# Optimization experiments

Hardware: AMD Instinct MI355X
Metric: run time of the kernel (lower is better)

The kernel has to match this reference:

```python
import jax, jax.numpy as jnp
import numpy as np

N = 50000       # nodes
E = 800000      # edges (before self-loops)
IN_DIM = 256
HID = 64
HEADS = 3
N_CLASSES = 40
NEG_SLOPE = 0.2  # PyG GATConv default negative_slope


def setup_inputs() -> dict:
    key = jax.random.key(0)
    ks = jax.random.split(key, 12)
    x = jax.random.normal(ks[0], (N, IN_DIM), jnp.float32)
    src = jax.random.randint(ks[1], (E,), 0, N, dtype=jnp.int32)
    off = jax.random.randint(ks[2], (E,), 1, N, dtype=jnp.int32)
    dst = (src + off) % N  # guarantees no self-loops
    edge_index = jnp.stack([src, dst], axis=0)
    g = 0.1
    W1 = jax.random.normal(ks[3], (IN_DIM, HEADS * HID), jnp.float32) * g
    att_src1 = jax.random.normal(ks[4], (HEADS, HID), jnp.float32) * g
    att_dst1 = jax.random.normal(ks[5], (HEADS, HID), jnp.float32) * g
    b1 = jnp.zeros((HEADS * HID,), jnp.float32)
    W2 = jax.random.normal(ks[6], (HEADS * HID, HEADS * HID), jnp.float32) * g
    att_src2 = jax.random.normal(ks[7], (HEADS, HID), jnp.float32) * g
    att_dst2 = jax.random.normal(ks[8], (HEADS, HID), jnp.float32) * g
    b2 = jnp.zeros((HEADS * HID,), jnp.float32)
    Wout = jax.random.normal(ks[9], (HEADS * HID, N_CLASSES), jnp.float32) * g
    bout = jnp.zeros((N_CLASSES,), jnp.float32)
    return {"x": x, "edge_index": edge_index,
            "W1": W1, "att_src1": att_src1, "att_dst1": att_dst1, "b1": b1,
            "W2": W2, "att_src2": att_src2, "att_dst2": att_dst2, "b2": b2,
            "Wout": Wout, "bout": bout}


def _segment_softmax(logits, seg, num_segments):
    # logits: [E', H], seg: [E'] destination node ids
    m = jax.ops.segment_max(logits, seg, num_segments=num_segments)
    e = jnp.exp(logits - m[seg])
    s = jax.ops.segment_sum(e, seg, num_segments=num_segments)
    return e / s[seg]


def _gat_layer(x, src, dst, W, att_src, att_dst, bias):
    n = x.shape[0]
    h = (x @ W).reshape(n, HEADS, HID)               # lin_src == lin_dst (x is a Tensor)
    a_src = jnp.sum(h * att_src, axis=-1)            # [N, H]
    a_dst = jnp.sum(h * att_dst, axis=-1)            # [N, H]
    alpha = jax.nn.leaky_relu(a_src[src] + a_dst[dst], NEG_SLOPE)  # [E', H]
    alpha = _segment_softmax(alpha, dst, n)
    msg = h[src] * alpha[:, :, None]                 # [E', H, C]
    out = jax.ops.segment_sum(msg, dst, num_segments=n)  # scatter-add aggregate
    return out.reshape(n, HEADS * HID) + bias        # concat heads + bias


def reference(x, edge_index, W1, att_src1, att_dst1, b1,
              W2, att_src2, att_dst2, b2, Wout, bout):
    n = x.shape[0]
    loop = jnp.arange(n, dtype=edge_index.dtype)
    src = jnp.concatenate([edge_index[0], loop])     # add_self_loops=True
    dst = jnp.concatenate([edge_index[1], loop])
    h = _gat_layer(x, src, dst, W1, att_src1, att_dst1, b1)
    h = jax.nn.relu(h)                               # dropout p=0 -> identity
    h = _gat_layer(h, src, dst, W2, att_src2, att_dst2, b2)
    h = jax.nn.relu(h)
    return h @ Wout + bout                           # node-level readout + outlayer
```

## Files before the change

### kernel.cpp

```cpp
#include <hip/hip_runtime.h>
#include <math.h>

#define NN 50000
#define NE 800000
#define KIN 256
#define F 192
#define NH 3
#define NC 40
#define NBLK 49

typedef unsigned short u16;
typedef unsigned int   u32;
typedef __attribute__((ext_vector_type(8))) short bf16x8;
typedef __attribute__((ext_vector_type(4))) float f32x4;

static __device__ __forceinline__ u16 f2bf(float f){
  u32 u = __float_as_uint(f);
  u32 r = (u + 0x7fffu + ((u >> 16) & 1u)) >> 16;
  return (u16)r;
}

__global__ void count_kernel(const int* __restrict__ dst, int* __restrict__ cnt){
  int e = blockIdx.x*256 + threadIdx.x;
  if (e < NE) atomicAdd(&cnt[dst[e]], 1);
}

__global__ __launch_bounds__(256) void partial_kernel(const int* __restrict__ cnt, int* __restrict__ partials){
  __shared__ int red[256];
  const int t = threadIdx.x;
  const int base = blockIdx.x*1024 + t*4;
  int s = 0;
  if (base + 3 < NN){
    int4 v = *(const int4*)&cnt[base];
    s = v.x + v.y + v.z + v.w;
  } else if (base < NN){
    for (int i=base; i<NN; i++) s += cnt[i];
  }
  red[t] = s;
  __syncthreads();
  for (int off=128; off; off>>=1){
    if (t < off) red[t] += red[t+off];
    __syncthreads();
  }
  if (t==0) partials[blockIdx.x] = red[0];
}

__global__ __launch_bounds__(64) void scan_partials(const int* __restrict__ partials,
                                                    int* __restrict__ offsets, int* __restrict__ row_ptr){
  const int lane = threadIdx.x;
  int p = (lane < NBLK)? partials[lane] : 0;
  int inc = p;
  #pragma unroll
  for (int off=1; off<64; off<<=1){
    int v = __shfl_up(inc, off);
    if (lane >= off) inc += v;
  }
  if (lane < NBLK) offsets[lane] = inc - p;
  if (lane == NBLK-1) row_ptr[NN] = inc;
}

__global__ __launch_bounds__(256) void emit_kernel(const int* __restrict__ cnt,
                                                   const int* __restrict__ offsets,
                                                   int* __restrict__ row_ptr){
  __shared__ int ts[256];
  const int t = threadIdx.x;
  const int base = blockIdx.x*1024 + t*4;
  int4 v = make_int4(0,0,0,0);
  if (base + 3 < NN) v = *(const int4*)&cnt[base];
  else if (base < NN){
    v.x = cnt[base];
    if (base+1 < NN) v.y = cnt[base+1];
    if (base+2 < NN) v.z = cnt[base+2];
  }
  int tot = v.x + v.y + v.z + v.w;
  ts[t] = tot;
  __syncthreads();
  #pragma unroll
  for (int off=1; off<256; off<<=1){
    int val = (t >= off)? ts[t-off] : 0;
    __syncthreads();
    ts[t] += val;
    __syncthreads();
  }
  int off0 = offsets[blockIdx.x] + ts[t] - tot;
  if (base < NN)     row_ptr[base]   = off0;
  if (base+1 < NN)   row_ptr[base+1] = off0 + v.x;
  if (base+2 < NN)   row_ptr[base+2] = off0 + v.x + v.y;
  if (base+3 < NN)   row_ptr[base+3] = off0 + v.x + v.y + v.z;
}

__global__ void fill_kernel(const int* __restrict__ src, const int* __restrict__ dst,
                            const int* __restrict__ row_ptr, int* __restrict__ cur,
                            int* __restrict__ col){
  int e = blockIdx.x*256 + threadIdx.x;
  if (e < NE){
    int d = dst[e];
    int p = row_ptr[d] + atomicAdd(&cur[d], 1);
    col[p] = src[e];
  }
}

__global__ void conv_x_kernel(const float* __restrict__ src, u16* __restrict__ dst, int n4){
  int i = blockIdx.x*256 + threadIdx.x;
  if (i < n4){
    float4 v = *(const float4*)&src[(size_t)i*4];
    uint2 p;
    p.x = (u32)f2bf(v.x) | ((u32)f2bf(v.y) << 16);
    p.y = (u32)f2bf(v.z) | ((u32)f2bf(v.w) << 16);
    *(uint2*)&dst[(size_t)i*4] = p;
  }
}

__global__ void conv_wt_kernel(const float* __restrict__ src, u16* __restrict__ dst, int R, int C){
  int e = blockIdx.x*256 + threadIdx.x;
  if (e < R*C){
    int r = e / C, c = e % C;
    dst[(size_t)c*R + r] = f2bf(src[e]);
  }
}

#define SAK 40
template<int K>
__global__ __launch_bounds__(256) void gemm_mfma(const u16* __restrict__ Ab, const u16* __restrict__ Bt,
                                                 u16* __restrict__ C,
                                                 const float* __restrict__ att_src, const float* __restrict__ att_dst,
                                                 float* __restrict__ a_src4, float* __restrict__ a_dst4){
  __shared__ __align__(16) u16 As[64*SAK];
  __shared__ __align__(16) u16 Bs[192*SAK];
  __shared__ float sd_src[64*NH];
  __shared__ float sd_dst[64*NH];
  const int t = threadIdx.x;
  const int wave = t >> 6, lane = t & 63;
  const int quad = lane >> 4, l16 = lane & 15;
  const int r0 = blockIdx.x*64;

  for (int i=t; i<64*NH; i+=256){ sd_src[i]=0.f; sd_dst[i]=0.f; }

  f32x4 acc[4][3];
  #pragma unroll
  for (int rt=0;rt<4;rt++)
    #pragma unroll
    for (int ct=0;ct<3;ct++) acc[rt][ct] = (f32x4){0.f,0.f,0.f,0.f};

  for (int k0=0; k0<K; k0+=32){
    __syncthreads();
    {
      int row = t >> 2, kq = t & 3;
      uint4 v = make_uint4(0,0,0,0);
      if (r0+row < NN) v = *(const uint4*)&Ab[(size_t)(r0+row)*K + k0 + kq*8];
      *(uint4*)&As[row*SAK + kq*8] = v;
    }
    #pragma unroll
    for (int i=0;i<3;i++){
      int idx = t + i*256;
      int n = idx >> 2, kq = idx & 3;
      *(uint4*)&Bs[n*SAK + kq*8] = *(const uint4*)&Bt[(size_t)n*K + k0 + kq*8];
    }
    __syncthreads();
    bf16x8 af[4], bf[3];
    #pragma unroll
    for (int rt=0;rt<4;rt++) af[rt] = *(const bf16x8*)&As[(rt*16 + l16)*SAK + quad*8];
    #pragma unroll
    for (int ct=0;ct<3;ct++) bf[ct] = *(const bf16x8*)&Bs[(wave*48 + ct*16 + l16)*SAK + quad*8];
    #pragma unroll
    for (int rt=0;rt<4;rt++)
      #pragma unroll
      for (int ct=0;ct<3;ct++)
        acc[rt][ct] = __builtin_amdgcn_mfma_f32_16x16x32_bf16(af[rt], bf[ct], acc[rt][ct], 0, 0, 0);
  }

  #pragma unroll
  for (int ct=0;ct<3;ct++){
    const int nbase = wave*48 + ct*16;
    const int n = nbase + l16;
    const int head = nbase >> 6;
    const float as_n = att_src[n], ad_n = att_dst[n];
    #pragma unroll
    for (int rt=0;rt<4;rt++){
      #pragma unroll
      for (int reg=0;reg<4;reg++){
        const int m = rt*16 + quad*4 + reg;
        const float v = acc[rt][ct][reg];
        const int grow = r0 + m;
        if (grow < NN) C[(size_t)grow*F + n] = f2bf(v);
        float ps = v*as_n, pd = v*ad_n;
        #pragma unroll
        for (int off=1; off<16; off<<=1){
          ps += __shfl_xor(ps, off);
          pd += __shfl_xor(pd, off);
        }
        if (l16 == 0){
          atomicAdd(&sd_src[m*NH + head], ps);
          atomicAdd(&sd_dst[m*NH + head], pd);
        }
      }
    }
  }
  __syncthreads();
  if (t < 64){
    int grow = r0 + t;
    if (grow < NN){
      float4 vs = make_float4(sd_src[t*NH+0], sd_src[t*NH+1], sd_src[t*NH+2], 0.f);
      float4 vd = make_float4(sd_dst[t*NH+0], sd_dst[t*NH+1], sd_dst[t*NH+2], 0.f);
      *(float4*)&a_src4[(size_t)grow*4] = vs;
      *(float4*)&a_dst4[(size_t)grow*4] = vd;
    }
  }
}

__global__ __launch_bounds__(256) void gat_agg_wave(const u16* __restrict__ hb,
    const float* __restrict__ a_src4, const float* __restrict__ a_dst4,
    const int* __restrict__ row_ptr, const int* __restrict__ col,
    const float* __restrict__ bias, u16* __restrict__ out){
  __shared__ float s_al[4][64][4];
  const int t = threadIdx.x;
  const int lane = t & 63;
  const int w = t >> 6;
  const int d = blockIdx.x*4 + w;
  if (d >= NN) return;
  const int e0  = row_ptr[d];
  const int deg = row_ptr[d+1] - e0;
  const int ecount = deg + 1;
  const float4 ad = *(const float4*)&a_dst4[(size_t)d*4];

  float m0=-1e30f, m1=-1e30f, m2=-1e30f;
  float s0=0.f, s1=0.f, s2=0.f;
  int   sn_r = d;
  float l0r=-1e30f, l1r=-1e30f, l2r=-1e30f;
  const int lastBase = ((ecount-1) >> 6) << 6;

  for (int base=0; base<ecount; base+=64){
    int j = base + lane;
    bool valid = j < ecount;
    int sn = d;
    if (j < deg) sn = col[e0+j];
    float4 as = *(const float4*)&a_src4[(size_t)sn*4];
    float l0 = as.x + ad.x; l0 = (l0>0.f)? l0 : 0.2f*l0;
    float l1 = as.y + ad.y; l1 = (l1>0.f)? l1 : 0.2f*l1;
    float l2 = as.z + ad.z; l2 = (l2>0.f)? l2 : 0.2f*l2;
    if (!valid){ l0=-1e30f; l1=-1e30f; l2=-1e30f; }
    float M0=l0, M1=l1, M2=l2;
    #pragma unroll
    for (int off=32; off; off>>=1){
      M0 = fmaxf(M0, __shfl_xor(M0, off));
      M1 = fmaxf(M1, __shfl_xor(M1, off));
      M2 = fmaxf(M2, __shfl_xor(M2, off));
    }
    float E0 = valid? __expf(l0-M0) : 0.f;
    float E1 = valid? __expf(l1-M1) : 0.f;
    float E2 = valid? __expf(l2-M2) : 0.f;
    float S0=E0, S1=E1, S2=E2;
    #pragma unroll
    for (int off=32; off; off>>=1){
      S0 += __shfl_xor(S0, off);
      S1 += __shfl_xor(S1, off);
      S2 += __shfl_xor(S2, off);
    }
    float n0 = fmaxf(m0,M0); s0 = s0*__expf(m0-n0) + S0*__expf(M0-n0); m0 = n0;
    float n1 = fmaxf(m1,M1); s1 = s1*__expf(m1-n1) + S1*__expf(M1-n1); m1 = n1;
    float n2 = fmaxf(m2,M2); s2 = s2*__expf(m2-n2) + S2*__expf(M2-n2); m2 = n2;
    sn_r = sn; l0r = l0; l1r = l1; l2r = l2;
  }
  const float i0 = 1.f/s0, i1 = 1.f/s1, i2 = 1.f/s2;

  const int cg = (lane < 48)? lane : lane - 48;
  const int hg = (lane < 48)? (lane >> 4) : (lane >> 4) - 3;
  const int cgo = cg*4;
  float4 acc = make_float4(0.f,0.f,0.f,0.f);
  for (int base=0; base<ecount; base+=64){
    int j = base + lane;
    bool valid = j < ecount;
    int sn; float l0,l1,l2;
    if (base == lastBase){ sn = sn_r; l0 = l0r; l1 = l1r; l2 = l2r; }
    else {
      sn = d;
      if (j < deg) sn = col[e0+j];
      float4 as = *(const float4*)&a_src4[(size_t)sn*4];
      l0 = as.x + ad.x; l0 = (l0>0.f)? l0 : 0.2f*l0;
      l1 = as.y + ad.y; l1 = (l1>0.f)? l1 : 0.2f*l1;
      l2 = as.z + ad.z; l2 = (l2>0.f)? l2 : 0.2f*l2;
    }
    float4 st;
    st.x = valid? __expf(l0-m0)*i0 : 0.f;
    st.y = valid? __expf(l1-m1)*i1 : 0.f;
    st.z = valid? __expf(l2-m2)*i2 : 0.f;
    st.w = 0.f;
    *(float4*)&s_al[w][lane][0] = st;
    __builtin_amdgcn_wave_barrier();
    int cnt = ecount - base; if (cnt > 64) cnt = 64;
    int jj = 0;
    for (; jj+4 <= cnt; jj += 4){
      int sA = __builtin_amdgcn_readlane(sn, jj);
      int sB = __builtin_amdgcn_readlane(sn, jj+1);
      int sC = __builtin_amdgcn_readlane(sn, jj+2);
      int sD = __builtin_amdgcn_readlane(sn, jj+3);
      uint2 pA = *(const uint2*)(hb + sA*F + cgo);
      uint2 pB = *(const uint2*)(hb + sB*F + cgo);
      uint2 pC = *(const uint2*)(hb + sC*F + cgo);
      uint2 pD = *(const uint2*)(hb + sD*F + cgo);
      float aA = s_al[w][jj  ][hg];
      float aB = s_al[w][jj+1][hg];
      float aC = s_al[w][jj+2][hg];
      float aD = s_al[w][jj+3][hg];
      acc.x = fmaf(aA, __uint_as_float(pA.x << 16),         acc.x);
      acc.y = fmaf(aA, __uint_as_float(pA.x & 0xffff0000u), acc.y);
      acc.z = fmaf(aA, __uint_as_float(pA.y << 16),         acc.z);
      acc.w = fmaf(aA, __uint_as_float(pA.y & 0xffff0000u), acc.w);
      acc.x = fmaf(aB, __uint_as_float(pB.x << 16),         acc.x);
      acc.y = fmaf(aB, __uint_as_float(pB.x & 0xffff0000u), acc.y);
      acc.z = fmaf(aB, __uint_as_float(pB.y << 16),         acc.z);
      acc.w = fmaf(aB, __uint_as_float(pB.y & 0xffff0000u), acc.w);
      acc.x = fmaf(aC, __uint_as_float(pC.x << 16),         acc.x);
      acc.y = fmaf(aC, __uint_as_float(pC.x & 0xffff0000u), acc.y);
      acc.z = fmaf(aC, __uint_as_float(pC.y << 16),         acc.z);
      acc.w = fmaf(aC, __uint_as_float(pC.y & 0xffff0000u), acc.w);
      acc.x = fmaf(aD, __uint_as_float(pD.x << 16),         acc.x);
      acc.y = fmaf(aD, __uint_as_float(pD.x & 0xffff0000u), acc.y);
      acc.z = fmaf(aD, __uint_as_float(pD.y << 16),         acc.z);
      acc.w = fmaf(aD, __uint_as_float(pD.y & 0xffff0000u), acc.w);
    }
    for (; jj < cnt; jj++){
      int sA = __builtin_amdgcn_readlane(sn, jj);
      uint2 pA = *(const uint2*)(hb + sA*F + cgo);
      float aA = s_al[w][jj][hg];
      acc.x = fmaf(aA, __uint_as_float(pA.x << 16),         acc.x);
      acc.y = fmaf(aA, __uint_as_float(pA.x & 0xffff0000u), acc.y);
      acc.z = fmaf(aA, __uint_as_float(pA.y << 16),         acc.z);
      acc.w = fmaf(aA, __uint_as_float(pA.y & 0xffff0000u), acc.w);
    }
    __builtin_amdgcn_wave_barrier();
  }
  if (lane < 48){
    float4 b4 = *(const float4*)&bias[cg*4];
    uint2 o;
    o.x = (u32)f2bf(fmaxf(acc.x + b4.x, 0.f)) | ((u32)f2bf(fmaxf(acc.y + b4.y, 0.f)) << 16);
    o.y = (u32)f2bf(fmaxf(acc.z + b4.z, 0.f)) | ((u32)f2bf(fmaxf(acc.w + b4.w, 0.f)) << 16);
    *(uint2*)&out[(size_t)d*F + cg*4] = o;
  }
}

#define SA 132
__global__ __launch_bounds__(256) void gemm_out_kernel(const u16* __restrict__ A,
    const float* __restrict__ W, const float* __restrict__ bias, float* __restrict__ C){
  __shared__ __align__(16) float As[32*SA];
  __shared__ float Ws[32*NC];
  const int t = threadIdx.x;
  const int tx = t & 7, ty = t >> 3;
  const int r0 = blockIdx.x*128;
  float acc[4][5];
  #pragma unroll
  for (int r=0;r<4;r++)
    #pragma unroll
    for (int c=0;c<5;c++) acc[r][c]=0.f;

  for (int k0=0; k0<F; k0+=32){
    __syncthreads();
    #pragma unroll
    for (int i=0;i<4;i++){
      int idx = t + i*256;
      int row = idx >> 3, kq = idx & 7;
      uint2 v = make_uint2(0,0);
      if (r0+row < NN) v = *(const uint2*)&A[(size_t)(r0+row)*F + k0 + kq*4];
      As[(kq*4+0)*SA + row] = __uint_as_float(v.x << 16);
      As[(kq*4+1)*SA + row] = __uint_as_float(v.x & 0xffff0000u);
      As[(kq*4+2)*SA + row] = __uint_as_float(v.y << 16);
      As[(kq*4+3)*SA + row] = __uint_as_float(v.y & 0xffff0000u);
    }
    #pragma unroll
    for (int i=0;i<5;i++){
      int idx = t + i*256;
      int k = idx/NC, c = idx%NC;
      Ws[k*NC + c] = W[(size_t)(k0+k)*NC + c];
    }
    __syncthreads();
    #pragma unroll
    for (int k=0;k<32;k++){
      float4 a = *(float4*)&As[k*SA + ty*4];
      float av[4] = {a.x,a.y,a.z,a.w};
      float bv[5];
      #pragma unroll
      for (int c=0;c<5;c++) bv[c] = Ws[k*NC + tx*5 + c];
      #pragma unroll
      for (int r=0;r<4;r++)
        #pragma unroll
        for (int c=0;c<5;c++) acc[r][c] = fmaf(av[r], bv[c], acc[r][c]);
    }
  }
  #pragma unroll
  for (int r=0;r<4;r++){
    int row = r0 + ty*4 + r;
    if (row < NN){
      #pragma unroll
      for (int c=0;c<5;c++) C[(size_t)row*NC + tx*5 + c] = acc[r][c] + bias[tx*5+c];
    }
  }
}

extern "C" void kernel_launch(void* const* d_in, const int* in_sizes, int n_in,
                              void* d_out, int out_size, void* d_ws, size_t ws_size,
                              hipStream_t stream){
  const float* x    = (const float*)d_in[0];
  const int*   ei   = (const int*)  d_in[1];
  const float* W1   = (const float*)d_in[2];
  const float* as1  = (const float*)d_in[3];
  const float* ad1  = (const float*)d_in[4];
  const float* b1   = (const float*)d_in[5];
  const float* W2   = (const float*)d_in[6];
  const float* as2  = (const float*)d_in[7];
  const float* ad2  = (const float*)d_in[8];
  const float* b2   = (const float*)d_in[9];
  const float* Wout = (const float*)d_in[10];
  const float* bout = (const float*)d_in[11];
  float* out = (float*)d_out;

  u16* xb  = (u16*)d_ws;
  u16* w1t = xb  + (size_t)NN*KIN;
  u16* w2t = w1t + (size_t)F*KIN;
  u16* hb1 = w2t + (size_t)F*F;
  u16* hb2 = hb1 + (size_t)NN*F;
  u16* gb1 = hb2 + (size_t)NN*F;
  u16* gb2 = gb1 + (size_t)NN*F;
  float* a_src4 = (float*)(gb2 + (size_t)NN*F);
  float* a_dst4 = a_src4 + (size_t)NN*4;
  int* row_ptr  = (int*)(a_dst4 + (size_t)NN*4);
  int* col      = row_ptr + (NN+1);
  int* cnt      = col + NE;
  int* partials = cnt + NN;
  int* offsets  = partials + NBLK;

  const int* srcv = ei;
  const int* dstv = ei + NE;

  hipMemsetAsync(cnt, 0, NN*sizeof(int), stream);
  count_kernel<<<(NE+255)/256, 256, 0, stream>>>(dstv, cnt);
  partial_kernel<<<NBLK, 256, 0, stream>>>(cnt, partials);
  scan_partials<<<1, 64, 0, stream>>>(partials, offsets, row_ptr);
  emit_kernel<<<NBLK, 256, 0, stream>>>(cnt, offsets, row_ptr);
  hipMemsetAsync(cnt, 0, NN*sizeof(int), stream);
  fill_kernel<<<(NE+255)/256, 256, 0, stream>>>(srcv, dstv, row_ptr, cnt, col);

  conv_x_kernel<<<(NN*KIN/4 + 255)/256, 256, 0, stream>>>(x, xb, NN*KIN/4);
  conv_wt_kernel<<<(KIN*F + 255)/256, 256, 0, stream>>>(W1, w1t, KIN, F);
  conv_wt_kernel<<<(F*F + 255)/256, 256, 0, stream>>>(W2, w2t, F, F);

  const int GEMM_GRID = (NN + 63)/64;
  const int AGG_GRID  = (NN + 3)/4;
  gemm_mfma<KIN><<<GEMM_GRID, 256, 0, stream>>>(xb, w1t, hb1, as1, ad1, a_src4, a_dst4);
  gat_agg_wave<<<AGG_GRID, 256, 0, stream>>>(hb1, a_src4, a_dst4, row_ptr, col, b1, gb1);
  gemm_mfma<F><<<GEMM_GRID, 256, 0, stream>>>(gb1, w2t, hb2, as2, ad2, a_src4, a_dst4);
  gat_agg_wave<<<AGG_GRID, 256, 0, stream>>>(hb2, a_src4, a_dst4, row_ptr, col, b2, gb2);
  gemm_out_kernel<<<(NN + 127)/128, 256, 0, stream>>>(gb2, Wout, bout, out);
}
```

Measured before the change: 414.2 us.

## Fuse x conversion into GEMM, stage epilogue via LDS, MFMA output layer

Several changes land together. The fp32-to-bf16 conversion of x now happens inside the first GEMM's A-tile load, which removes a separate pass over x. The GEMM epilogue stages the bf16 tile in shared memory, so stores are coalesced and the attention dot products are computed per row and head, replacing shuffle reductions and LDS atomics. The output FC layer now uses MFMA with a transposed, padded bf16 Wout. The count reset is folded into emit_kernel, which drops one memset. The first GEMM now reads twice as many bytes for A per tile, and attention logits are computed from bf16-rounded values.

```diff
diff --git a/kernel.cpp b/kernel.cpp
--- a/kernel.cpp
+++ b/kernel.cpp
@@ -59,7 +59,7 @@
   if (lane == NBLK-1) row_ptr[NN] = inc;
 }
 
-__global__ __launch_bounds__(256) void emit_kernel(const int* __restrict__ cnt,
+__global__ __launch_bounds__(256) void emit_kernel(int* __restrict__ cnt,
                                                    const int* __restrict__ offsets,
                                                    int* __restrict__ row_ptr){
   __shared__ int ts[256];
@@ -83,10 +83,17 @@
     __syncthreads();
   }
   int off0 = offsets[blockIdx.x] + ts[t] - tot;
-  if (base < NN)     row_ptr[base]   = off0;
-  if (base+1 < NN)   row_ptr[base+1] = off0 + v.x;
-  if (base+2 < NN)   row_ptr[base+2] = off0 + v.x + v.y;
-  if (base+3 < NN)   row_ptr[base+3] = off0 + v.x + v.y + v.z;
+  if (base + 3 < NN){
+    row_ptr[base]   = off0;
+    row_ptr[base+1] = off0 + v.x;
+    row_ptr[base+2] = off0 + v.x + v.y;
+    row_ptr[base+3] = off0 + v.x + v.y + v.z;
+    *(int4*)&cnt[base] = make_int4(0,0,0,0);
+  } else if (base < NN){
+    row_ptr[base] = off0; cnt[base] = 0;
+    if (base+1 < NN){ row_ptr[base+1] = off0 + v.x; cnt[base+1] = 0; }
+    if (base+2 < NN){ row_ptr[base+2] = off0 + v.x + v.y; cnt[base+2] = 0; }
+  }
 }
 
 __global__ void fill_kernel(const int* __restrict__ src, const int* __restrict__ dst,
@@ -100,17 +107,6 @@
   }
 }
 
-__global__ void conv_x_kernel(const float* __restrict__ src, u16* __restrict__ dst, int n4){
-  int i = blockIdx.x*256 + threadIdx.x;
-  if (i < n4){
-    float4 v = *(const float4*)&src[(size_t)i*4];
-    uint2 p;
-    p.x = (u32)f2bf(v.x) | ((u32)f2bf(v.y) << 16);
-    p.y = (u32)f2bf(v.z) | ((u32)f2bf(v.w) << 16);
-    *(uint2*)&dst[(size_t)i*4] = p;
-  }
-}
-
 __global__ void conv_wt_kernel(const float* __restrict__ src, u16* __restrict__ dst, int R, int C){
   int e = blockIdx.x*256 + threadIdx.x;
   if (e < R*C){
@@ -119,23 +115,30 @@
   }
 }
 
+__global__ void conv_wout_kernel(const float* __restrict__ W, u16* __restrict__ dst){
+  int e = blockIdx.x*256 + threadIdx.x;
+  if (e < 48*F){
+    int n = e / F, k = e % F;
+    dst[e] = (n < NC)? f2bf(W[(size_t)k*NC + n]) : (u16)0;
+  }
+}
+
 #define SAK 40
-template<int K>
-__global__ __launch_bounds__(256) void gemm_mfma(const u16* __restrict__ Ab, const u16* __restrict__ Bt,
+#define SC  196
+template<int K, bool CONVA>
+__global__ __launch_bounds__(256) void gemm_mfma(const void* __restrict__ Araw, const u16* __restrict__ Bt,
                                                  u16* __restrict__ C,
                                                  const float* __restrict__ att_src, const float* __restrict__ att_dst,
                                                  float* __restrict__ a_src4, float* __restrict__ a_dst4){
-  __shared__ __align__(16) u16 As[64*SAK];
-  __shared__ __align__(16) u16 Bs[192*SAK];
-  __shared__ float sd_src[64*NH];
-  __shared__ float sd_dst[64*NH];
+  __shared__ __align__(16) union {
+    struct { u16 As[64*SAK]; u16 Bs[192*SAK]; } st;
+    u16 Cs[64*SC];
+  } sh;
   const int t = threadIdx.x;
   const int wave = t >> 6, lane = t & 63;
   const int quad = lane >> 4, l16 = lane & 15;
   const int r0 = blockIdx.x*64;
 
-  for (int i=t; i<64*NH; i+=256){ sd_src[i]=0.f; sd_dst[i]=0.f; }
-
   f32x4 acc[4][3];
   #pragma unroll
   for (int rt=0;rt<4;rt++)
@@ -146,22 +149,38 @@
     __syncthreads();
     {
       int row = t >> 2, kq = t & 3;
-      uint4 v = make_uint4(0,0,0,0);
-      if (r0+row < NN) v = *(const uint4*)&Ab[(size_t)(r0+row)*K + k0 + kq*8];
-      *(uint4*)&As[row*SAK + kq*8] = v;
+      if (CONVA){
+        const float* Af = (const float*)Araw;
+        float4 v0 = make_float4(0.f,0.f,0.f,0.f), v1 = make_float4(0.f,0.f,0.f,0.f);
+        if (r0+row < NN){
+          v0 = *(const float4*)&Af[(size_t)(r0+row)*K + k0 + kq*8];
+          v1 = *(const float4*)&Af[(size_t)(r0+row)*K + k0 + kq*8 + 4];
+        }
+        uint4 p;
+        p.x = (u32)f2bf(v0.x) | ((u32)f2bf(v0.y) << 16);
+        p.y = (u32)f2bf(v0.z) | ((u32)f2bf(v0.w) << 16);
+        p.z = (u32)f2bf(v1.x) | ((u32)f2bf(v1.y) << 16);
+        p.w = (u32)f2bf(v1.z) | ((u32)f2bf(v1.w) << 16);
+        *(uint4*)&sh.st.As[row*SAK + kq*8] = p;
+      } else {
+        const u16* Ab = (const u16*)Araw;
+        uint4 v = make_uint4(0,0,0,0);
+        if (r0+row < NN) v = *(const uint4*)&Ab[(size_t)(r0+row)*K + k0 + kq*8];
+        *(uint4*)&sh.st.As[row*SAK + kq*8] = v;
+      }
     }
     #pragma unroll
     for (int i=0;i<3;i++){
       int idx = t + i*256;
       int n = idx >> 2, kq = idx & 3;
-      *(uint4*)&Bs[n*SAK + kq*8] = *(const uint4*)&Bt[(size_t)n*K + k0 + kq*8];
+      *(uint4*)&sh.st.Bs[n*SAK + kq*8] = *(const uint4*)&Bt[(size_t)n*K + k0 + kq*8];
     }
     __syncthreads();
     bf16x8 af[4], bf[3];
     #pragma unroll
-    for (int rt=0;rt<4;rt++) af[rt] = *(const bf16x8*)&As[(rt*16 + l16)*SAK + quad*8];
-    #pragma unroll
-    for (int ct=0;ct<3;ct++) bf[ct] = *(const bf16x8*)&Bs[(wave*48 + ct*16 + l16)*SAK + quad*8];
+    for (int rt=0;rt<4;rt++) af[rt] = *(const bf16x8*)&sh.st.As[(rt*16 + l16)*SAK + quad*8];
+    #pragma unroll
+    for (int ct=0;ct<3;ct++) bf[ct] = *(const bf16x8*)&sh.st.Bs[(wave*48 + ct*16 + l16)*SAK + quad*8];
     #pragma unroll
     for (int rt=0;rt<4;rt++)
       #pragma unroll
@@ -169,41 +188,55 @@
         acc[rt][ct] = __builtin_amdgcn_mfma_f32_16x16x32_bf16(af[rt], bf[ct], acc[rt][ct], 0, 0, 0);
   }
 
+  __syncthreads();
   #pragma unroll
   for (int ct=0;ct<3;ct++){
-    const int nbase = wave*48 + ct*16;
-    const int n = nbase + l16;
-    const int head = nbase >> 6;
-    const float as_n = att_src[n], ad_n = att_dst[n];
+    const int n = wave*48 + ct*16 + l16;
     #pragma unroll
     for (int rt=0;rt<4;rt++){
       #pragma unroll
       for (int reg=0;reg<4;reg++){
         const int m = rt*16 + quad*4 + reg;
-        const float v = acc[rt][ct][reg];
-        const int grow = r0 + m;
-        if (grow < NN) C[(size_t)grow*F + n] = f2bf(v);
-        float ps = v*as_n, pd = v*ad_n;
-        #pragma unroll
-        for (int off=1; off<16; off<<=1){
-          ps += __shfl_xor(ps, off);
-          pd += __shfl_xor(pd, off);
-        }
-        if (l16 == 0){
-          atomicAdd(&sd_src[m*NH + head], ps);
-          atomicAdd(&sd_dst[m*NH + head], pd);
-        }
+        sh.Cs[m*SC + n] = f2bf(acc[rt][ct][reg]);
       }
     }
   }
   __syncthreads();
-  if (t < 64){
-    int grow = r0 + t;
+  {
+    int row = t >> 2, c0 = (t & 3)*6;
+    int grow = r0 + row;
     if (grow < NN){
-      float4 vs = make_float4(sd_src[t*NH+0], sd_src[t*NH+1], sd_src[t*NH+2], 0.f);
-      float4 vd = make_float4(sd_dst[t*NH+0], sd_dst[t*NH+1], sd_dst[t*NH+2], 0.f);
-      *(float4*)&a_src4[(size_t)grow*4] = vs;
-      *(float4*)&a_dst4[(size_t)grow*4] = vd;
+      #pragma unroll
+      for (int j=0;j<6;j++){
+        int ch = c0 + j;
+        uint4 v = *(const uint4*)&sh.Cs[row*SC + ch*8];
+        *(uint4*)&C[(size_t)grow*F + ch*8] = v;
+      }
+    }
+  }
+  if (t < 192){
+    int row = t & 63, head = t >> 6;
+    int grow = r0 + row;
+    if (grow < NN){
+      float ps = 0.f, pd = 0.f;
+      #pragma unroll
+      for (int j=0;j<8;j++){
+        uint4 v = *(const uint4*)&sh.Cs[row*SC + head*64 + j*8];
+        float4 w0 = *(const float4*)&att_src[head*64 + j*8];
+        float4 w1 = *(const float4*)&att_src[head*64 + j*8 + 4];
+        float4 d0 = *(const float4*)&att_dst[head*64 + j*8];
+        float4 d1 = *(const float4*)&att_dst[head*64 + j*8 + 4];
+        float c0f = __uint_as_float(v.x << 16), c1f = __uint_as_float(v.x & 0xffff0000u);
+        float c2f = __uint_as_float(v.y << 16), c3f = __uint_as_float(v.y & 0xffff0000u);
+        float c4f = __uint_as_float(v.z << 16), c5f = __uint_as_float(v.z & 0xffff0000u);
+        float c6f = __uint_as_float(v.w << 16), c7f = __uint_as_float(v.w & 0xffff0000u);
+        ps = fmaf(c0f,w0.x,fmaf(c1f,w0.y,fmaf(c2f,w0.z,fmaf(c3f,w0.w,ps))));
+        ps = fmaf(c4f,w1.x,fmaf(c5f,w1.y,fmaf(c6f,w1.z,fmaf(c7f,w1.w,ps))));
+        pd = fmaf(c0f,d0.x,fmaf(c1f,d0.y,fmaf(c2f,d0.z,fmaf(c3f,d0.w,pd))));
+        pd = fmaf(c4f,d1.x,fmaf(c5f,d1.y,fmaf(c6f,d1.z,fmaf(c7f,d1.w,pd))));
+      }
+      a_src4[(size_t)grow*4 + head] = ps;
+      a_dst4[(size_t)grow*4 + head] = pd;
     }
   }
 }
@@ -339,59 +372,36 @@
   }
 }
 
-#define SA 132
-__global__ __launch_bounds__(256) void gemm_out_kernel(const u16* __restrict__ A,
-    const float* __restrict__ W, const float* __restrict__ bias, float* __restrict__ C){
-  __shared__ __align__(16) float As[32*SA];
-  __shared__ float Ws[32*NC];
+__global__ __launch_bounds__(256) void gemm_out_mfma(const u16* __restrict__ A,
+    const u16* __restrict__ Wt, const float* __restrict__ bias, float* __restrict__ out){
   const int t = threadIdx.x;
-  const int tx = t & 7, ty = t >> 3;
-  const int r0 = blockIdx.x*128;
-  float acc[4][5];
-  #pragma unroll
-  for (int r=0;r<4;r++)
-    #pragma unroll
-    for (int c=0;c<5;c++) acc[r][c]=0.f;
-
-  for (int k0=0; k0<F; k0+=32){
-    __syncthreads();
-    #pragma unroll
-    for (int i=0;i<4;i++){
-      int idx = t + i*256;
-      int row = idx >> 3, kq = idx & 7;
-      uint2 v = make_uint2(0,0);
-      if (r0+row < NN) v = *(const uint2*)&A[(size_t)(r0+row)*F + k0 + kq*4];
-      As[(kq*4+0)*SA + row] = __uint_as_float(v.x << 16);
-      As[(kq*4+1)*SA + row] = __uint_as_float(v.x & 0xffff0000u);
-      As[(kq*4+2)*SA + row] = __uint_as_float(v.y << 16);
-      As[(kq*4+3)*SA + row] = __uint_as_float(v.y & 0xffff0000u);
-    }
-    #pragma unroll
-    for (int i=0;i<5;i++){
-      int idx = t + i*256;
-      int k = idx/NC, c = idx%NC;
-      Ws[k*NC + c] = W[(size_t)(k0+k)*NC + c];
-    }
-    __syncthreads();
-    #pragma unroll
-    for (int k=0;k<32;k++){
-      float4 a = *(float4*)&As[k*SA + ty*4];
-      float av[4] = {a.x,a.y,a.z,a.w};
-      float bv[5];
-      #pragma unroll
-      for (int c=0;c<5;c++) bv[c] = Ws[k*NC + tx*5 + c];
-      #pragma unroll
-      for (int r=0;r<4;r++)
-        #pragma unroll
-        for (int c=0;c<5;c++) acc[r][c] = fmaf(av[r], bv[c], acc[r][c]);
-    }
-  }
-  #pragma unroll
-  for (int r=0;r<4;r++){
-    int row = r0 + ty*4 + r;
-    if (row < NN){
-      #pragma unroll
-      for (int c=0;c<5;c++) C[(size_t)row*NC + tx*5 + c] = acc[r][c] + bias[tx*5+c];
+  const int wave = t >> 6, lane = t & 63;
+  const int quad = lane >> 4, l16 = lane & 15;
+  const int rbase = blockIdx.x*64 + wave*16;
+  const int arow = rbase + l16;
+  f32x4 acc[3];
+  #pragma unroll
+  for (int ct=0;ct<3;ct++) acc[ct] = (f32x4){0.f,0.f,0.f,0.f};
+  #pragma unroll
+  for (int ks=0; ks<6; ks++){
+    const int k0 = ks*32;
+    union { uint4 u; bf16x8 h; } cva;
+    cva.u = make_uint4(0,0,0,0);
+    if (arow < NN) cva.u = *(const uint4*)&A[(size_t)arow*F + k0 + quad*8];
+    #pragma unroll
+    for (int ct=0;ct<3;ct++){
+      bf16x8 bfr = *(const bf16x8*)&Wt[(size_t)(ct*16 + l16)*F + k0 + quad*8];
+      acc[ct] = __builtin_amdgcn_mfma_f32_16x16x32_bf16(cva.h, bfr, acc[ct], 0, 0, 0);
+    }
+  }
+  #pragma unroll
+  for (int ct=0;ct<3;ct++){
+    const int n = ct*16 + l16;
+    #pragma unroll
+    for (int reg=0;reg<4;reg++){
+      const int m = quad*4 + reg;
+      const int grow = rbase + m;
+      if (grow < NN && n < NC) out[(size_t)grow*NC + n] = acc[ct][reg] + bias[n];
     }
   }
 }
@@ -413,10 +423,10 @@
   const float* bout = (const float*)d_in[11];
   float* out = (float*)d_out;
 
-  u16* xb  = (u16*)d_ws;
-  u16* w1t = xb  + (size_t)NN*KIN;
+  u16* w1t = (u16*)d_ws;
   u16* w2t = w1t + (size_t)F*KIN;
-  u16* hb1 = w2t + (size_t)F*F;
+  u16* wot = w2t + (size_t)F*F;
+  u16* hb1 = wot + (size_t)48*F;
   u16* hb2 = hb1 + (size_t)NN*F;
   u16* gb1 = hb2 + (size_t)NN*F;
   u16* gb2 = gb1 + (size_t)NN*F;
@@ -436,18 +446,17 @@
   partial_kernel<<<NBLK, 256, 0, stream>>>(cnt, partials);
   scan_partials<<<1, 64, 0, stream>>>(partials, offsets, row_ptr);
   emit_kernel<<<NBLK, 256, 0, stream>>>(cnt, offsets, row_ptr);
-  hipMemsetAsync(cnt, 0, NN*sizeof(int), stream);
   fill_kernel<<<(NE+255)/256, 256, 0, stream>>>(srcv, dstv, row_ptr, cnt, col);
 
-  conv_x_kernel<<<(NN*KIN/4 + 255)/256, 256, 0, stream>>>(x, xb, NN*KIN/4);
   conv_wt_kernel<<<(KIN*F + 255)/256, 256, 0, stream>>>(W1, w1t, KIN, F);
   conv_wt_kernel<<<(F*F + 255)/256, 256, 0, stream>>>(W2, w2t, F, F);
+  conv_wout_kernel<<<(48*F + 255)/256, 256, 0, stream>>>(Wout, wot);
 
   const int GEMM_GRID = (NN + 63)/64;
   const int AGG_GRID  = (NN + 3)/4;
-  gemm_mfma<KIN><<<GEMM_GRID, 256, 0, stream>>>(xb, w1t, hb1, as1, ad1, a_src4, a_dst4);
+  gemm_mfma<KIN,true><<<GEMM_GRID, 256, 0, stream>>>(x, w1t, hb1, as1, ad1, a_src4, a_dst4);
   gat_agg_wave<<<AGG_GRID, 256, 0, stream>>>(hb1, a_src4, a_dst4, row_ptr, col, b1, gb1);
-  gemm_mfma<F><<<GEMM_GRID, 256, 0, stream>>>(gb1, w2t, hb2, as2, ad2, a_src4, a_dst4);
+  gemm_mfma<F,false><<<GEMM_GRID, 256, 0, stream>>>(gb1, w2t, hb2, as2, ad2, a_src4, a_dst4);
   gat_agg_wave<<<AGG_GRID, 256, 0, stream>>>(hb2, a_src4, a_dst4, row_ptr, col, b2, gb2);
-  gemm_out_kernel<<<(NN + 127)/128, 256, 0, stream>>>(gb2, Wout, bout, out);
-}
+  gemm_out_mfma<<<GEMM_GRID, 256, 0, stream>>>(gb2, wot, bout, out);
+}
```

Result: faster. 363.5 us (-12.2%).
